# Kernel optimization log

Hardware: AMD Instinct MI355X
Metric: run time of the kernel (lower is better)

Reference implementation:

```python
import jax, jax.numpy as jnp
import numpy as np

B, S, D = 2, 2048, 2048
N_HEADS, N_KV_HEADS, HEAD_DIM = 16, 8, 128
N_REP = N_HEADS // N_KV_HEADS
EPS = 1e-6
SCALE = HEAD_DIM ** -0.5


def setup_inputs() -> dict:
    key = jax.random.key(0)
    ks = jax.random.split(key, 6)
    x = jax.random.normal(ks[0], (B, S, D), dtype=jnp.float32)
    # RoPE frequencies (Llama-style cis stored as interleaved [cos, sin])
    inv_freq = 1.0 / (1e6 ** (jnp.arange(0, HEAD_DIM, 2, dtype=jnp.float32) / HEAD_DIM))
    angles = jnp.arange(S, dtype=jnp.float32)[:, None] * inv_freq[None, :]  # [S, HEAD_DIM//2]
    freqs_cis = jnp.stack([jnp.cos(angles), jnp.sin(angles)], axis=-1)  # [S, HEAD_DIM//2, 2]
    wq = jax.random.normal(ks[1], (N_HEADS * HEAD_DIM, D), dtype=jnp.float32) * 0.02
    wk = jax.random.normal(ks[2], (N_KV_HEADS * HEAD_DIM, D), dtype=jnp.float32) * 0.02
    wv = jax.random.normal(ks[3], (N_KV_HEADS * HEAD_DIM, D), dtype=jnp.float32) * 0.02
    wo = jax.random.normal(ks[4], (D, N_HEADS * HEAD_DIM), dtype=jnp.float32) * 0.02
    q_norm_w = jnp.ones((HEAD_DIM,), dtype=jnp.float32)
    k_norm_w = jnp.ones((HEAD_DIM,), dtype=jnp.float32)
    return {"x": x, "freqs_cis": freqs_cis, "wq": wq, "wk": wk, "wv": wv,
            "wo": wo, "q_norm_w": q_norm_w, "k_norm_w": k_norm_w}


def _rmsnorm(t, w):
    var = jnp.mean(jnp.square(t), axis=-1, keepdims=True)
    return t * jax.lax.rsqrt(var + EPS) * w


def _apply_rope(t, cos, sin):
    # t: [B, S, H, HEAD_DIM]; cos/sin: [1, S, 1, HEAD_DIM//2]
    tp = t.reshape(*t.shape[:-1], HEAD_DIM // 2, 2)
    tr, ti = tp[..., 0], tp[..., 1]
    out = jnp.stack([tr * cos - ti * sin, tr * sin + ti * cos], axis=-1)
    return out.reshape(t.shape)


def reference(x, freqs_cis, wq, wk, wv, wo, q_norm_w, k_norm_w):
    bs, seqlen, _ = x.shape
    xq = (x @ wq.T).reshape(bs, seqlen, N_HEADS, HEAD_DIM)
    xk = (x @ wk.T).reshape(bs, seqlen, N_KV_HEADS, HEAD_DIM)
    xv = (x @ wv.T).reshape(bs, seqlen, N_KV_HEADS, HEAD_DIM)
    # per-head RMSNorm (Qwen3)
    xq = _rmsnorm(xq, q_norm_w)
    xk = _rmsnorm(xk, k_norm_w)
    # rotary embedding
    cos = freqs_cis[:seqlen, :, 0][None, :, None, :]
    sin = freqs_cis[:seqlen, :, 1][None, :, None, :]
    xq = _apply_rope(xq, cos, sin)
    xk = _apply_rope(xk, cos, sin)
    # GQA: repeat kv heads
    keys = jnp.repeat(xk, N_REP, axis=2)    # [B, S, N_HEADS, HEAD_DIM]
    values = jnp.repeat(xv, N_REP, axis=2)
    q = xq.transpose(0, 2, 1, 3)   # [B, H, S, D]
    k = keys.transpose(0, 2, 1, 3)
    v = values.transpose(0, 2, 1, 3)
    scores = jnp.einsum("bhqd,bhkd->bhqk", q, k) * SCALE
    causal = jnp.tril(jnp.ones((seqlen, seqlen), dtype=bool))
    scores = jnp.where(causal[None, None], scores, jnp.finfo(scores.dtype).min)
    attn = jax.nn.softmax(scores, axis=-1)
    out = jnp.einsum("bhqk,bhkd->bhqd", attn, v)
    out = out.transpose(0, 2, 1, 3).reshape(bs, seqlen, N_HEADS * HEAD_DIM)
    return out @ wo.T
```

## Files before the change

kernel.cpp:

```cpp
#include <hip/hip_runtime.h>

#define B_ 2
#define S_ 2048
#define D_ 2048
#define NH 16
#define NKV 8
#define HD 128
#define SCALE 0.08838834764831845f
#define CEXP 0.1275255f
#define RTHR 62.733f

typedef unsigned short u16;
typedef __attribute__((ext_vector_type(8))) short short8;
typedef __attribute__((ext_vector_type(4))) float f32x4;
typedef __attribute__((ext_vector_type(16))) float f32x16;
typedef __attribute__((ext_vector_type(4))) int i32x4;
typedef __attribute__((ext_vector_type(2))) int i32x2;

#define ASM_VMCNT(N) asm volatile("s_waitcnt vmcnt(" #N ")" ::: "memory")
#define MEMFENCE asm volatile("" ::: "memory")

__device__ __forceinline__ u16 f2b(float f) {
  union { float f; unsigned u; } c; c.f = f;
  unsigned u = c.u;
  return (u16)((u + 0x7fffu + ((u >> 16) & 1u)) >> 16);
}
__device__ __forceinline__ float b2f(u16 h) {
  union { unsigned u; float f; } c; c.u = ((unsigned)h) << 16;
  return c.f;
}
__device__ __forceinline__ float exp2f_fast(float x) {
  float r; asm("v_exp_f32 %0, %1" : "=v"(r) : "v"(x)); return r;
}
__device__ __forceinline__ int cvtpk(float a, float b) {
  int r; asm("v_cvt_pk_bf16_f32 %0, %1, %2" : "=v"(r) : "v"(a), "v"(b)); return r;
}
__device__ __forceinline__ void pl32swap(int& a, int& b) {
  asm volatile("v_permlane32_swap_b32 %0, %1" : "+v"(a), "+v"(b));
}

__device__ __forceinline__ void load_lds16(const u16* g, u16* l) {
  __builtin_amdgcn_global_load_lds(
      (const __attribute__((address_space(1))) unsigned int*)g,
      (__attribute__((address_space(3))) unsigned int*)l, 16, 0, 0);
}

__global__ __launch_bounds__(256) void cvt_all(const float* __restrict__ x,
                                               const float* __restrict__ wq,
                                               const float* __restrict__ wk,
                                               const float* __restrict__ wv,
                                               const float* __restrict__ wo,
                                               u16* __restrict__ xb,
                                               u16* __restrict__ wqkvb,
                                               u16* __restrict__ wob) {
  const int blk = blockIdx.x;
  const float* src; u16* dst; int base;
  if (blk < 8192)       { src = x;  dst = xb;                  base = blk; }
  else if (blk < 12288) { src = wq; dst = wqkvb;               base = blk - 8192; }
  else if (blk < 14336) { src = wk; dst = wqkvb + 2048 * 2048; base = blk - 12288; }
  else if (blk < 16384) { src = wv; dst = wqkvb + 3072 * 2048; base = blk - 14336; }
  else                  { src = wo; dst = wob;                 base = blk - 16384; }
  int i = base * 256 + threadIdx.x;
  float4 v = ((const float4*)src)[i];
  u16 o0 = f2b(v.x), o1 = f2b(v.y), o2 = f2b(v.z), o3 = f2b(v.w);
  unsigned long long packed = (unsigned long long)o0 | ((unsigned long long)o1 << 16) |
                              ((unsigned long long)o2 << 32) | ((unsigned long long)o3 << 48);
  ((unsigned long long*)dst)[i] = packed;
}

__global__ __launch_bounds__(256, 4) void gemm_qkv_fused2(const u16* __restrict__ A,
                                                          const u16* __restrict__ Bm,
                                                          const float* __restrict__ fc,
                                                          const float* __restrict__ qw,
                                                          const float* __restrict__ kw,
                                                          u16* __restrict__ qrope,
                                                          u16* __restrict__ krope,
                                                          u16* __restrict__ vt) {
  __shared__ __align__(16) u16 As[128 * 64];
  __shared__ __align__(16) u16 Bs[128 * 64];
  __shared__ float sq[2][128];
  const int tid = threadIdx.x;
  const int wave = tid >> 6, lane = tid & 63;
  const int L = (blockIdx.x & 7) * 128 + (blockIdx.x >> 3);
  const int bm = L >> 5, bn = L & 31;
  const int wr = wave >> 1, wc = wave & 1;
  const int r = lane & 15, hi = lane >> 4;

  f32x4 acc[4][4];
#pragma unroll
  for (int mi = 0; mi < 4; ++mi)
#pragma unroll
    for (int ni = 0; ni < 4; ++ni) acc[mi][ni] = (f32x4){0.f, 0.f, 0.f, 0.f};

  const int gslot = (lane & 7) ^ (lane >> 3);
  const int srow = lane >> 3;

  auto stage = [&](int k0) {
#pragma unroll
    for (int jj = 0; jj < 4; ++jj) {
      int j = wave * 4 + jj;
      int row = j * 8 + srow;
      load_lds16(A + (size_t)(bm * 128 + row) * 2048 + k0 + gslot * 8, &As[j * 512]);
      load_lds16(Bm + (size_t)(bn * 128 + row) * 2048 + k0 + gslot * 8, &Bs[j * 512]);
    }
  };

  for (int kt = 0; kt < 32; ++kt) {
    stage(kt << 6);
    ASM_VMCNT(0);
    __builtin_amdgcn_s_barrier();
    MEMFENCE;
#pragma unroll
    for (int kc = 0; kc < 2; ++kc) {
      short8 af[4], bfr[4];
#pragma unroll
      for (int m = 0; m < 4; ++m) {
        int row = wr * 64 + m * 16 + r;
        int slot = (hi + kc * 4) ^ (row & 7);
        af[m] = *(const short8*)&As[row * 64 + slot * 8];
      }
#pragma unroll
      for (int n = 0; n < 4; ++n) {
        int row = wc * 64 + n * 16 + r;
        int slot = (hi + kc * 4) ^ (row & 7);
        bfr[n] = *(const short8*)&Bs[row * 64 + slot * 8];
      }
      __builtin_amdgcn_s_setprio(1);
#pragma unroll
      for (int m = 0; m < 4; ++m)
#pragma unroll
        for (int n = 0; n < 4; ++n)
          acc[m][n] = __builtin_amdgcn_mfma_f32_16x16x32_bf16(af[m], bfr[n], acc[m][n], 0, 0, 0);
      __builtin_amdgcn_s_setprio(0);
    }
    MEMFENCE;
    __builtin_amdgcn_s_barrier();
  }

  if (bn >= 24) {
    const int hv = bn - 24;
#pragma unroll
    for (int mi = 0; mi < 4; ++mi) {
      const int tok0 = bm * 128 + wr * 64 + mi * 16 + hi * 4;
      const int bb = tok0 >> 11, sl = tok0 & 2047;
#pragma unroll
      for (int ni = 0; ni < 4; ++ni) {
        const int d = wc * 64 + ni * 16 + r;
        int w0 = cvtpk(acc[mi][ni][0], acc[mi][ni][1]);
        int w1 = cvtpk(acc[mi][ni][2], acc[mi][ni][3]);
        i32x2 pk = (i32x2){w0, w1};
        *(i32x2*)(vt + ((size_t)(bb * 8 + hv) * 128 + d) * 2048 + sl) = pk;
      }
    }
  } else {
    const float* nw = (bn < 16) ? qw : kw;
    float nwv[4];
#pragma unroll
    for (int ni = 0; ni < 4; ++ni) nwv[ni] = nw[wc * 64 + ni * 16 + r];
    float ssq[4][4];
#pragma unroll
    for (int mi = 0; mi < 4; ++mi)
#pragma unroll
      for (int r2 = 0; r2 < 4; ++r2) {
        float s4 = 0.f;
#pragma unroll
        for (int ni = 0; ni < 4; ++ni) {
          float a = acc[mi][ni][r2];
          s4 = __builtin_fmaf(a, a, s4);
        }
#pragma unroll
        for (int mk = 1; mk < 16; mk <<= 1) s4 += __shfl_xor(s4, mk, 64);
        ssq[mi][r2] = s4;
      }
    if (r == 0) {
#pragma unroll
      for (int mi = 0; mi < 4; ++mi)
#pragma unroll
        for (int r2 = 0; r2 < 4; ++r2)
          sq[wc][wr * 64 + mi * 16 + hi * 4 + r2] = ssq[mi][r2];
    }
    __syncthreads();
    u16* outp = (bn < 16) ? qrope : krope;
#pragma unroll
    for (int mi = 0; mi < 4; ++mi) {
      const int tok0 = bm * 128 + wr * 64 + mi * 16 + hi * 4;
      const int bb = tok0 >> 11;
      const size_t headbase = (bn < 16) ? ((size_t)(bb * 16 + bn) * 2048)
                                        : ((size_t)(bb * 8 + (bn - 16)) * 2048);
#pragma unroll
      for (int r2 = 0; r2 < 4; ++r2) {
        const int sl = (tok0 + r2) & 2047;
        const float tot = ssq[mi][r2] + sq[wc ^ 1][wr * 64 + mi * 16 + hi * 4 + r2];
        const float rms = rsqrtf(tot * (1.0f / 128.0f) + 1e-6f);
#pragma unroll
        for (int ni = 0; ni < 4; ++ni) {
          const int d = wc * 64 + ni * 16 + r;
          float val = acc[mi][ni][r2] * rms * nwv[ni];
          float prt = __shfl_xor(val, 1, 64);
          const float2 cs = *(const float2*)&fc[(size_t)(sl * 64 + (d >> 1)) * 2];
          float outv = (r & 1) ? (prt * cs.y + val * cs.x)
                               : (val * cs.x - prt * cs.y);
          outp[(headbase + sl) * 128 + d] = f2b(outv);
        }
      }
    }
  }
}

template<int OUTF32>
__global__ __launch_bounds__(256, 4) void gemm_bt3(const u16* __restrict__ A, const u16* __restrict__ Bm,
                                                   void* __restrict__ Cv, int M, int N, int K, int nbn) {
  __shared__ __align__(16) u16 As[128 * 64];
  __shared__ __align__(16) u16 Bs[128 * 64];
  const int tid = threadIdx.x;
  const int wave = tid >> 6, lane = tid & 63;
  const int nwg = gridDim.x, cpx = nwg >> 3;
  const int L = (blockIdx.x & 7) * cpx + (blockIdx.x >> 3);
  const int bm = L / nbn, bn = L % nbn;
  const int wr = wave >> 1, wc = wave & 1;
  const int r = lane & 15, hi = lane >> 4;

  f32x4 acc[4][4];
#pragma unroll
  for (int m = 0; m < 4; ++m)
#pragma unroll
    for (int n = 0; n < 4; ++n) acc[m][n] = (f32x4){0.f, 0.f, 0.f, 0.f};

  const int gslot = (lane & 7) ^ (lane >> 3);
  const int srow = lane >> 3;

  auto stage = [&](int k0) {
#pragma unroll
    for (int jj = 0; jj < 4; ++jj) {
      int j = wave * 4 + jj;
      int row = j * 8 + srow;
      load_lds16(A + (size_t)(bm * 128 + row) * K + k0 + gslot * 8, &As[j * 512]);
      load_lds16(Bm + (size_t)(bn * 128 + row) * K + k0 + gslot * 8, &Bs[j * 512]);
    }
  };

  const int nk = K >> 6;
  for (int kt = 0; kt < nk; ++kt) {
    stage(kt << 6);
    ASM_VMCNT(0);
    __builtin_amdgcn_s_barrier();
    MEMFENCE;
#pragma unroll
    for (int kc = 0; kc < 2; ++kc) {
      short8 af[4], bfr[4];
#pragma unroll
      for (int m = 0; m < 4; ++m) {
        int row = wr * 64 + m * 16 + r;
        int slot = (hi + kc * 4) ^ (row & 7);
        af[m] = *(const short8*)&As[row * 64 + slot * 8];
      }
#pragma unroll
      for (int n = 0; n < 4; ++n) {
        int row = wc * 64 + n * 16 + r;
        int slot = (hi + kc * 4) ^ (row & 7);
        bfr[n] = *(const short8*)&Bs[row * 64 + slot * 8];
      }
#pragma unroll
      for (int m = 0; m < 4; ++m)
#pragma unroll
        for (int n = 0; n < 4; ++n)
          acc[m][n] = __builtin_amdgcn_mfma_f32_16x16x32_bf16(af[m], bfr[n], acc[m][n], 0, 0, 0);
    }
    MEMFENCE;
    __builtin_amdgcn_s_barrier();
  }

#pragma unroll
  for (int m = 0; m < 4; ++m)
#pragma unroll
    for (int n = 0; n < 4; ++n)
#pragma unroll
      for (int r2 = 0; r2 < 4; ++r2) {
        int grow = bm * 128 + wr * 64 + m * 16 + hi * 4 + r2;
        int gcol = bn * 128 + wc * 64 + n * 16 + r;
        if (OUTF32)
          ((float*)Cv)[(size_t)grow * N + gcol] = acc[m][n][r2];
        else
          ((u16*)Cv)[(size_t)grow * N + gcol] = f2b(acc[m][n][r2]);
      }
}

__global__ __launch_bounds__(256, 2) void attn9(const u16* __restrict__ qr, const u16* __restrict__ kr,
                                                const u16* __restrict__ vt, u16* __restrict__ ao) {
  __shared__ __align__(16) u16 Ks[2][64 * 128];
  __shared__ __align__(16) u16 Vs[2][128 * 64];
  const int tid = threadIdx.x, wave = tid >> 6, lane = tid & 63;
  const int ql = lane & 31, lh = lane >> 5;

  const int blk = blockIdx.x;
  const int half = blk >> 8;
  const int xcd = blk & 7;
  const int idx = (blk >> 3) & 31;
  const int bh = xcd * 4 + (idx & 3);
  const int pp = idx >> 2;
  const int t = half ? pp : 15 - pp;
  const int b = bh >> 4, h = bh & 15, hkv = h >> 1;

  const u16* Q  = qr + (size_t)(b * 16 + h) * S_ * HD;
  const u16* Kg = kr + (size_t)(b * 8 + hkv) * S_ * HD;
  const u16* Vg = vt + (size_t)(b * 8 + hkv) * HD * S_;

  const int q0w = t * 128 + wave * 32;
  const int nsteps = 2 * (t + 1);

  short8 qf[8];
#pragma unroll
  for (int ki = 0; ki < 8; ++ki)
    qf[ki] = *(const short8*)(Q + (size_t)(q0w + ql) * HD + ki * 16 + lh * 8);

  f32x16 o[4];
#pragma unroll
  for (int dt = 0; dt < 4; ++dt) o[dt] = 0.f;
  float m = -1e30f, l = 0.f;

  auto stage = [&](int buf, int kv0) {
#pragma unroll
    for (int inst = 0; inst < 4; ++inst) {
      int pp2 = wave * 4096 + inst * 1024 + lane * 16;
      int row = pp2 >> 8;
      int colb = (pp2 & 255) ^ ((row & 7) << 4);
      load_lds16(Kg + (((size_t)(kv0 + row)) << 7) + (colb >> 1),
                 &Ks[buf][(wave * 4096 + inst * 1024) >> 1]);
    }
#pragma unroll
    for (int inst = 0; inst < 4; ++inst) {
      int pp2 = wave * 4096 + inst * 1024 + lane * 16;
      int d = pp2 >> 7;
      int colb = (pp2 & 127) ^ ((d & 7) << 4);
      load_lds16(Vg + (size_t)d * S_ + kv0 + (colb >> 1),
                 &Vs[buf][(wave * 4096 + inst * 1024) >> 1]);
    }
  };

  stage(0, 0);
  for (int i = 0; i < nsteps; ++i) {
    const int kv0 = i * 64;
    const u16* kb = Ks[i & 1];
    const u16* vb = Vs[i & 1];

    ASM_VMCNT(0);
    __builtin_amdgcn_s_barrier();
    MEMFENCE;
    if (i + 1 < nsteps) stage((i + 1) & 1, kv0 + 64);

    if (kv0 < q0w + 32) {
      f32x16 sacc[2];
      sacc[0] = 0.f; sacc[1] = 0.f;
      __builtin_amdgcn_s_setprio(1);
#pragma unroll
      for (int ki = 0; ki < 8; ++ki) {
        const int off = ki * 32 + lh * 16;
#pragma unroll
        for (int kvt = 0; kvt < 2; ++kvt) {
          const int row = kvt * 32 + ql;
          short8 kf = *(const short8*)&kb[(row << 7) + ((off ^ ((row & 7) << 4)) >> 1)];
          sacc[kvt] = __builtin_amdgcn_mfma_f32_32x32x16_bf16(kf, qf[ki], sacc[kvt], 0, 0, 0);
        }
      }
      __builtin_amdgcn_s_setprio(0);
      const int q = q0w + ql;
      if (kv0 + 64 > q0w) {
#pragma unroll
        for (int kvt = 0; kvt < 2; ++kvt) {
          const int kvb = kv0 + kvt * 32 + 4 * lh;
#pragma unroll
          for (int reg = 0; reg < 16; ++reg) {
            const int kvr = kvb + (reg & 3) + 8 * (reg >> 2);
            sacc[kvt][reg] = (kvr > q) ? -1e30f : sacc[kvt][reg];
          }
        }
      }
      float mx = sacc[0][0];
#pragma unroll
      for (int kvt = 0; kvt < 2; ++kvt)
#pragma unroll
        for (int reg = 0; reg < 16; ++reg) mx = fmaxf(mx, sacc[kvt][reg]);
      mx = fmaxf(mx, __shfl_xor(mx, 32, 64));
      if (__any(mx > m + RTHR)) {
        float mn = fmaxf(m, mx);
        float sc = exp2f_fast((m - mn) * CEXP);
        l *= sc;
        m = mn;
#pragma unroll
        for (int dt = 0; dt < 4; ++dt)
#pragma unroll
          for (int reg = 0; reg < 16; ++reg) o[dt][reg] *= sc;
      }
      short8 pf[4];
      const float mc = m * CEXP;
      float ps = 0.f;
#pragma unroll
      for (int kvt = 0; kvt < 2; ++kvt) {
        float pv[16];
#pragma unroll
        for (int reg = 0; reg < 16; ++reg) {
          pv[reg] = exp2f_fast(__builtin_fmaf(sacc[kvt][reg], CEXP, -mc));
          ps += pv[reg];
        }
        int A0 = cvtpk(pv[0], pv[1]),  B0 = cvtpk(pv[2], pv[3]);
        int C0 = cvtpk(pv[4], pv[5]),  D0 = cvtpk(pv[6], pv[7]);
        int A1 = cvtpk(pv[8], pv[9]),  B1 = cvtpk(pv[10], pv[11]);
        int C1 = cvtpk(pv[12], pv[13]), D1 = cvtpk(pv[14], pv[15]);
        pl32swap(A0, C0);
        pl32swap(B0, D0);
        pl32swap(A1, C1);
        pl32swap(B1, D1);
        i32x4 w0 = (i32x4){A0, B0, C0, D0};
        i32x4 w1 = (i32x4){A1, B1, C1, D1};
        pf[kvt * 2]     = *(short8*)&w0;
        pf[kvt * 2 + 1] = *(short8*)&w1;
      }
      l += ps;
      __builtin_amdgcn_s_setprio(1);
#pragma unroll
      for (int kc = 0; kc < 4; ++kc) {
        const int off = kc * 32 + lh * 16;
#pragma unroll
        for (int dt = 0; dt < 4; ++dt) {
          const int d = dt * 32 + ql;
          short8 vf = *(const short8*)&vb[(d << 6) + ((off ^ ((d & 7) << 4)) >> 1)];
          o[dt] = __builtin_amdgcn_mfma_f32_32x32x16_bf16(vf, pf[kc], o[dt], 0, 0, 0);
        }
      }
      __builtin_amdgcn_s_setprio(0);
    }
    MEMFENCE;
  }

  l += __shfl_xor(l, 32, 64);
  const float inv = 1.0f / l;
  const size_t rowoff = ((size_t)(b * 2048 + q0w + ql)) * 2048 + h * 128;
#pragma unroll
  for (int dt = 0; dt < 4; ++dt)
#pragma unroll
    for (int g = 0; g < 4; ++g) {
      const int d0 = dt * 32 + 8 * g + 4 * lh;
      int w0 = cvtpk(o[dt][4 * g] * inv, o[dt][4 * g + 1] * inv);
      int w1 = cvtpk(o[dt][4 * g + 2] * inv, o[dt][4 * g + 3] * inv);
      i32x2 pk = (i32x2){w0, w1};
      *(i32x2*)((u16*)ao + rowoff + d0) = pk;
    }
}

extern "C" void kernel_launch(void* const* d_in, const int* in_sizes, int n_in,
                              void* d_out, int out_size, void* d_ws, size_t ws_size,
                              hipStream_t stream) {
  const float* x = (const float*)d_in[0];
  const float* fc = (const float*)d_in[1];
  const float* wq = (const float*)d_in[2];
  const float* wk = (const float*)d_in[3];
  const float* wv = (const float*)d_in[4];
  const float* wo = (const float*)d_in[5];
  const float* qw = (const float*)d_in[6];
  const float* kw = (const float*)d_in[7];
  float* out = (float*)d_out;
  char* ws = (char*)d_ws;

  u16* xb    = (u16*)(ws);
  u16* wqkvb = (u16*)(ws + 16777216);
  u16* wob   = (u16*)(ws + 33554432);
  u16* qrope = (u16*)(ws + 75497472);
  u16* krope = (u16*)(ws + 92274688);
  u16* vtb   = (u16*)(ws + 100663296);
  u16* ao    = (u16*)(ws + 109051904);

  cvt_all<<<20480, 256, 0, stream>>>(x, wq, wk, wv, wo, xb, wqkvb, wob);

  gemm_qkv_fused2<<<1024, 256, 0, stream>>>(xb, wqkvb, fc, qw, kw, qrope, krope, vtb);

  attn9<<<512, 256, 0, stream>>>(qrope, krope, vtb, ao);

  gemm_bt3<1><<<512, 256, 0, stream>>>(ao, wob, (void*)out, 4096, 2048, 2048, 16);
}
```

Baseline: 199.5 us.

## Rewrite QKV GEMM as 256x256 tile double-buffered 8-phase pipeline

The fused QKV projection kernel moves from 128x128 tiles with 256 threads and a single LDS buffer to 256x256 tiles with 512 threads (8 waves) and double-buffered LDS. The K loop is split into eight phases. Each phase stages a half-tile of the next K slice while MFMAs run on a quarter of the current tile, so global loads overlap compute and operand reuse per tile is higher. The norm/RoPE and V-transpose epilogue is remapped so each block covers two heads. In exchange, it uses roughly 132KB of LDS per block and launches only 256 blocks, which limits occupancy and tail balancing.

```diff
diff --git a/kernel.cpp b/kernel.cpp
--- a/kernel.cpp
+++ b/kernel.cpp
@@ -68,98 +68,123 @@
   ((unsigned long long*)dst)[i] = packed;
 }
 
-__global__ __launch_bounds__(256, 4) void gemm_qkv_fused2(const u16* __restrict__ A,
-                                                          const u16* __restrict__ Bm,
-                                                          const float* __restrict__ fc,
-                                                          const float* __restrict__ qw,
-                                                          const float* __restrict__ kw,
-                                                          u16* __restrict__ qrope,
-                                                          u16* __restrict__ krope,
-                                                          u16* __restrict__ vt) {
-  __shared__ __align__(16) u16 As[128 * 64];
-  __shared__ __align__(16) u16 Bs[128 * 64];
-  __shared__ float sq[2][128];
+__device__ __forceinline__ short8 ldfrag(const u16* buf, int grow, int kc, int hi) {
+  return *(const short8*)&buf[grow * 64 + kc * 32 + ((hi ^ ((grow >> 1) & 3)) << 3)];
+}
+
+__global__ __launch_bounds__(512, 2) void gemm_qkv_8ph(const u16* __restrict__ A,
+                                                       const u16* __restrict__ Bm,
+                                                       const float* __restrict__ fc,
+                                                       const float* __restrict__ qw,
+                                                       const float* __restrict__ kw,
+                                                       u16* __restrict__ qrope,
+                                                       u16* __restrict__ krope,
+                                                       u16* __restrict__ vt) {
+  __shared__ __align__(16) u16 As[2][16384];
+  __shared__ __align__(16) u16 Bs[2][16384];
+  __shared__ float sq[4][256];
   const int tid = threadIdx.x;
   const int wave = tid >> 6, lane = tid & 63;
-  const int L = (blockIdx.x & 7) * 128 + (blockIdx.x >> 3);
-  const int bm = L >> 5, bn = L & 31;
-  const int wr = wave >> 1, wc = wave & 1;
+  const int L = (blockIdx.x & 7) * 32 + (blockIdx.x >> 3);
+  const int bm = L >> 4, bn = L & 15;
+  const int wr = wave >> 2, wc = wave & 3;
   const int r = lane & 15, hi = lane >> 4;
-
-  f32x4 acc[4][4];
-#pragma unroll
-  for (int mi = 0; mi < 4; ++mi)
+  const int rowA0 = bm * 256, rowB0 = bn * 256;
+
+  f32x4 acc[8][4];
+#pragma unroll
+  for (int mi = 0; mi < 8; ++mi)
 #pragma unroll
     for (int ni = 0; ni < 4; ++ni) acc[mi][ni] = (f32x4){0.f, 0.f, 0.f, 0.f};
 
-  const int gslot = (lane & 7) ^ (lane >> 3);
-  const int srow = lane >> 3;
-
-  auto stage = [&](int k0) {
-#pragma unroll
-    for (int jj = 0; jj < 4; ++jj) {
-      int j = wave * 4 + jj;
-      int row = j * 8 + srow;
-      load_lds16(A + (size_t)(bm * 128 + row) * 2048 + k0 + gslot * 8, &As[j * 512]);
-      load_lds16(Bm + (size_t)(bn * 128 + row) * 2048 + k0 + gslot * 8, &Bs[j * 512]);
+  auto stage_half = [&](const u16* G, int rowbase, u16* buf, int half, int kcol) {
+#pragma unroll
+    for (int l = 0; l < 2; ++l) {
+      const int p = wave * 2048 + l * 1024 + lane * 16;
+      const int row = p >> 7;
+      const int slot16 = (p >> 4) & 7;
+      const int kc = slot16 >> 2, sl = slot16 & 3;
+      const int lrow = half * 128 + row;
+      const int kg = sl ^ ((lrow >> 1) & 3);
+      load_lds16(G + (size_t)(rowbase + lrow) * 2048 + kcol + kc * 32 + kg * 8,
+                 (u16*)((char*)buf + half * 16384 + wave * 2048 + l * 1024));
     }
   };
 
-  for (int kt = 0; kt < 32; ++kt) {
-    stage(kt << 6);
-    ASM_VMCNT(0);
-    __builtin_amdgcn_s_barrier();
-    MEMFENCE;
-#pragma unroll
-    for (int kc = 0; kc < 2; ++kc) {
-      short8 af[4], bfr[4];
-#pragma unroll
-      for (int m = 0; m < 4; ++m) {
-        int row = wr * 64 + m * 16 + r;
-        int slot = (hi + kc * 4) ^ (row & 7);
-        af[m] = *(const short8*)&As[row * 64 + slot * 8];
-      }
-#pragma unroll
-      for (int n = 0; n < 4; ++n) {
-        int row = wc * 64 + n * 16 + r;
-        int slot = (hi + kc * 4) ^ (row & 7);
-        bfr[n] = *(const short8*)&Bs[row * 64 + slot * 8];
-      }
-      __builtin_amdgcn_s_setprio(1);
-#pragma unroll
-      for (int m = 0; m < 4; ++m)
-#pragma unroll
-        for (int n = 0; n < 4; ++n)
-          acc[m][n] = __builtin_amdgcn_mfma_f32_16x16x32_bf16(af[m], bfr[n], acc[m][n], 0, 0, 0);
-      __builtin_amdgcn_s_setprio(0);
-    }
-    MEMFENCE;
-    __builtin_amdgcn_s_barrier();
+#define PHASEQ(BUFA, BUFB, MH, NH, STMT, VM) \
+  { STMT; VM; \
+    MEMFENCE; __builtin_amdgcn_s_barrier(); MEMFENCE; \
+    short8 afq[4][2], bfq[2][2]; \
+    _Pragma("unroll") for (int i2 = 0; i2 < 4; ++i2) { \
+      afq[i2][0] = ldfrag(BUFA, wr * 128 + MH * 64 + i2 * 16 + r, 0, hi); \
+      afq[i2][1] = ldfrag(BUFA, wr * 128 + MH * 64 + i2 * 16 + r, 1, hi); } \
+    _Pragma("unroll") for (int j2 = 0; j2 < 2; ++j2) { \
+      bfq[j2][0] = ldfrag(BUFB, wc * 64 + NH * 32 + j2 * 16 + r, 0, hi); \
+      bfq[j2][1] = ldfrag(BUFB, wc * 64 + NH * 32 + j2 * 16 + r, 1, hi); } \
+    __builtin_amdgcn_s_setprio(1); \
+    _Pragma("unroll") for (int i2 = 0; i2 < 4; ++i2) \
+    _Pragma("unroll") for (int j2 = 0; j2 < 2; ++j2) { \
+      acc[MH * 4 + i2][NH * 2 + j2] = __builtin_amdgcn_mfma_f32_16x16x32_bf16( \
+          afq[i2][0], bfq[j2][0], acc[MH * 4 + i2][NH * 2 + j2], 0, 0, 0); \
+      acc[MH * 4 + i2][NH * 2 + j2] = __builtin_amdgcn_mfma_f32_16x16x32_bf16( \
+          afq[i2][1], bfq[j2][1], acc[MH * 4 + i2][NH * 2 + j2], 0, 0, 0); } \
+    __builtin_amdgcn_s_setprio(0); \
+    MEMFENCE; __builtin_amdgcn_s_barrier(); MEMFENCE; }
+
+  stage_half(A,  rowA0, As[0], 0, 0);
+  stage_half(A,  rowA0, As[0], 1, 0);
+  stage_half(Bm, rowB0, Bs[0], 0, 0);
+  stage_half(Bm, rowB0, Bs[0], 1, 0);
+  ASM_VMCNT(0);
+  __builtin_amdgcn_s_barrier();
+  MEMFENCE;
+
+  for (int i = 0; i < 16; ++i) {
+    const int kc1 = (2 * i + 1) << 6;
+    const int kc2 = (2 * i + 2) << 6;
+    const bool hn = i + 1 < 16;
+    PHASEQ(As[0], Bs[0], 0, 0, stage_half(A,  rowA0, As[1], 0, kc1), ASM_VMCNT(2));
+    PHASEQ(As[0], Bs[0], 0, 1, stage_half(A,  rowA0, As[1], 1, kc1), );
+    PHASEQ(As[0], Bs[0], 1, 0, stage_half(Bm, rowB0, Bs[1], 0, kc1), );
+    PHASEQ(As[0], Bs[0], 1, 1, stage_half(Bm, rowB0, Bs[1], 1, kc1), );
+    if (hn) {
+      PHASEQ(As[1], Bs[1], 0, 0, stage_half(A,  rowA0, As[0], 0, kc2), ASM_VMCNT(2));
+      PHASEQ(As[1], Bs[1], 0, 1, stage_half(A,  rowA0, As[0], 1, kc2), );
+      PHASEQ(As[1], Bs[1], 1, 0, stage_half(Bm, rowB0, Bs[0], 0, kc2), );
+      PHASEQ(As[1], Bs[1], 1, 1, stage_half(Bm, rowB0, Bs[0], 1, kc2), );
+    } else {
+      PHASEQ(As[1], Bs[1], 0, 0, , ASM_VMCNT(0));
+      PHASEQ(As[1], Bs[1], 0, 1, , );
+      PHASEQ(As[1], Bs[1], 1, 0, , );
+      PHASEQ(As[1], Bs[1], 1, 1, , );
+    }
   }
 
-  if (bn >= 24) {
-    const int hv = bn - 24;
-#pragma unroll
-    for (int mi = 0; mi < 4; ++mi) {
-      const int tok0 = bm * 128 + wr * 64 + mi * 16 + hi * 4;
+  const int headg = 2 * bn + (wc >> 1);
+  if (bn >= 12) {
+    const int hv = headg - 24;
+#pragma unroll
+    for (int mi = 0; mi < 8; ++mi) {
+      const int tok0 = bm * 256 + wr * 128 + mi * 16 + hi * 4;
       const int bb = tok0 >> 11, sl = tok0 & 2047;
 #pragma unroll
       for (int ni = 0; ni < 4; ++ni) {
-        const int d = wc * 64 + ni * 16 + r;
+        const int dh = (wc & 1) * 64 + ni * 16 + r;
         int w0 = cvtpk(acc[mi][ni][0], acc[mi][ni][1]);
         int w1 = cvtpk(acc[mi][ni][2], acc[mi][ni][3]);
         i32x2 pk = (i32x2){w0, w1};
-        *(i32x2*)(vt + ((size_t)(bb * 8 + hv) * 128 + d) * 2048 + sl) = pk;
+        *(i32x2*)(vt + ((size_t)(bb * 8 + hv) * 128 + dh) * 2048 + sl) = pk;
       }
     }
   } else {
-    const float* nw = (bn < 16) ? qw : kw;
+    const bool isq = bn < 8;
+    const float* nw = isq ? qw : kw;
     float nwv[4];
 #pragma unroll
-    for (int ni = 0; ni < 4; ++ni) nwv[ni] = nw[wc * 64 + ni * 16 + r];
-    float ssq[4][4];
-#pragma unroll
-    for (int mi = 0; mi < 4; ++mi)
+    for (int ni = 0; ni < 4; ++ni) nwv[ni] = nw[(wc & 1) * 64 + ni * 16 + r];
+    float ssq[8][4];
+#pragma unroll
+    for (int mi = 0; mi < 8; ++mi)
 #pragma unroll
       for (int r2 = 0; r2 < 4; ++r2) {
         float s4 = 0.f;
@@ -174,33 +199,34 @@
       }
     if (r == 0) {
 #pragma unroll
-      for (int mi = 0; mi < 4; ++mi)
+      for (int mi = 0; mi < 8; ++mi)
 #pragma unroll
         for (int r2 = 0; r2 < 4; ++r2)
-          sq[wc][wr * 64 + mi * 16 + hi * 4 + r2] = ssq[mi][r2];
+          sq[wc][wr * 128 + mi * 16 + hi * 4 + r2] = ssq[mi][r2];
     }
     __syncthreads();
-    u16* outp = (bn < 16) ? qrope : krope;
-#pragma unroll
-    for (int mi = 0; mi < 4; ++mi) {
-      const int tok0 = bm * 128 + wr * 64 + mi * 16 + hi * 4;
+    u16* outp = isq ? qrope : krope;
+    const int hb = isq ? headg : headg - 16;
+    const int hmod = isq ? 16 : 8;
+#pragma unroll
+    for (int mi = 0; mi < 8; ++mi) {
+      const int tok0 = bm * 256 + wr * 128 + mi * 16 + hi * 4;
       const int bb = tok0 >> 11;
-      const size_t headbase = (bn < 16) ? ((size_t)(bb * 16 + bn) * 2048)
-                                        : ((size_t)(bb * 8 + (bn - 16)) * 2048);
+      const size_t headbase = (size_t)(bb * hmod + hb) * 2048;
 #pragma unroll
       for (int r2 = 0; r2 < 4; ++r2) {
         const int sl = (tok0 + r2) & 2047;
-        const float tot = ssq[mi][r2] + sq[wc ^ 1][wr * 64 + mi * 16 + hi * 4 + r2];
+        const float tot = ssq[mi][r2] + sq[wc ^ 1][wr * 128 + mi * 16 + hi * 4 + r2];
         const float rms = rsqrtf(tot * (1.0f / 128.0f) + 1e-6f);
 #pragma unroll
         for (int ni = 0; ni < 4; ++ni) {
-          const int d = wc * 64 + ni * 16 + r;
+          const int dh = (wc & 1) * 64 + ni * 16 + r;
           float val = acc[mi][ni][r2] * rms * nwv[ni];
           float prt = __shfl_xor(val, 1, 64);
-          const float2 cs = *(const float2*)&fc[(size_t)(sl * 64 + (d >> 1)) * 2];
+          const float2 cs = *(const float2*)&fc[(size_t)(sl * 64 + (dh >> 1)) * 2];
           float outv = (r & 1) ? (prt * cs.y + val * cs.x)
                                : (val * cs.x - prt * cs.y);
-          outp[(headbase + sl) * 128 + d] = f2b(outv);
+          outp[(headbase + sl) * 128 + dh] = f2b(outv);
         }
       }
     }
@@ -471,7 +497,7 @@
 
   cvt_all<<<20480, 256, 0, stream>>>(x, wq, wk, wv, wo, xb, wqkvb, wob);
 
-  gemm_qkv_fused2<<<1024, 256, 0, stream>>>(xb, wqkvb, fc, qw, kw, qrope, krope, vtb);
+  gemm_qkv_8ph<<<256, 512, 0, stream>>>(xb, wqkvb, fc, qw, kw, qrope, krope, vtb);
 
   attn9<<<512, 256, 0, stream>>>(qrope, krope, vtb, ao);
 
```

Measured after the change: 342.8 us. +71.8%, slower.
